# Kernel tuning notes

Measured on AMD Instinct MI355X. Metric: run time of the kernel, lower is better.

The kernel has to match this reference:

```python
import jax, jax.numpy as jnp
import numpy as np

NUM_THRESH = 1000


def setup_inputs() -> dict:
    key = jax.random.key(0)
    k1, k2 = jax.random.split(key)
    B, C, H, W = 16, 4, 512, 512
    inp = jax.random.uniform(k1, (B, C, H, W), dtype=jnp.float32)
    targ = (jax.random.uniform(k2, (B, C, H, W)) < 0.3).astype(jnp.float32)
    return {"input": inp, "target": targ}


def _max_f1_loss(input, target):
    # input, target: [B, C, H, W]; loss = mean_c (1 - max_t F1_c(t))
    B, C, H, W = input.shape
    N = B * H * W
    x = jnp.transpose(input, (1, 0, 2, 3)).reshape(C, N)   # [C, N]
    y = jnp.transpose(target, (1, 0, 2, 3)).reshape(C, N)  # [C, N]
    thresholds = jnp.linspace(0.0, 1.0, NUM_THRESH).astype(jnp.float32)

    def per_class(xc, yc):
        # idx[n] = number of thresholds strictly below xc[n]  (in [0, 1000])
        # sample n is predicted positive (xc > t_k) exactly for k < idx[n]
        idx = jnp.searchsorted(thresholds, xc, side='left')
        s_y = jax.ops.segment_sum(yc, idx, num_segments=NUM_THRESH + 1)
        s_1 = jax.ops.segment_sum(jnp.ones_like(yc), idx, num_segments=NUM_THRESH + 1)
        cum_y = jnp.cumsum(s_y)[:NUM_THRESH]  # sum of y over samples with idx <= k
        cum_1 = jnp.cumsum(s_1)[:NUM_THRESH]
        total_y = jnp.sum(yc)
        TP = total_y - cum_y            # sum(target * pred) per threshold
        PP = jnp.float32(N) - cum_1     # sum(pred) per threshold
        FP = PP - TP                    # sum((1-target) * pred)
        FN = total_y - TP               # sum(target * (1-pred))
        denom = TP + (FN + FP) * 0.5
        F1 = jnp.where(denom == 0, 0.0, TP / jnp.where(denom == 0, 1.0, denom))
        return 1.0 - jnp.max(F1)

    losses = jax.vmap(per_class)(x, y)  # [C]
    return jnp.mean(losses)


def reference(input, target):
    return _max_f1_loss(input, target)
```

## Files before the change

kernel.cpp:

```cpp
#include <hip/hip_runtime.h>

#define NBINS 1001
#define HIST_BLOCK 1024
#define ELEMS_PER_BLOCK 32768

__device__ __forceinline__ int bin_of(float v) {
    int k = (int)ceilf(v * 999.0f);
    k = (k < 0) ? 0 : k;
    k = (k > 1000) ? 1000 : k;
    return k;
}

__global__ __launch_bounds__(HIST_BLOCK, 4) void hist_kernel(
    const float* __restrict__ x, const float* __restrict__ y,
    unsigned long long* __restrict__ ghist, int HW)
{
    __shared__ unsigned int lh[2][NBINS];
    const int tid = threadIdx.x;
    if (tid < NBINS) { lh[0][tid] = 0u; lh[1][tid] = 0u; }
    __syncthreads();

    const long long start = (long long)blockIdx.x * ELEMS_PER_BLOCK;
    const int c = (int)((start / HW) & 3);

    const float4* __restrict__ x4 = (const float4*)(x + start);
    const float4* __restrict__ y4 = (const float4*)(y + start);

    unsigned int* __restrict__ h = lh[(tid >> 6) & 1];

    #pragma unroll
    for (int r = 0; r < 2; ++r) {
        float4 xv[4], yv[4];
        #pragma unroll
        for (int k = 0; k < 4; ++k) {
            const int idx = (r * 4 + k) * HIST_BLOCK + tid;
            xv[k] = x4[idx];
            yv[k] = y4[idx];
        }
        #pragma unroll
        for (int k = 0; k < 4; ++k) {
            atomicAdd(&h[bin_of(xv[k].x)], 1u + ((__float_as_uint(yv[k].x) >> 8) & 0x10000u));
            atomicAdd(&h[bin_of(xv[k].y)], 1u + ((__float_as_uint(yv[k].y) >> 8) & 0x10000u));
            atomicAdd(&h[bin_of(xv[k].z)], 1u + ((__float_as_uint(yv[k].z) >> 8) & 0x10000u));
            atomicAdd(&h[bin_of(xv[k].w)], 1u + ((__float_as_uint(yv[k].w) >> 8) & 0x10000u));
        }
    }
    __syncthreads();

    if (tid < NBINS) {
        unsigned int v = lh[0][tid] + lh[1][tid];
        if (v) {
            unsigned long long add = (unsigned long long)(v & 0xffffu)
                                   | ((unsigned long long)(v >> 16) << 32);
            atomicAdd(&ghist[(size_t)c * NBINS + tid], add);
        }
    }
}

__global__ __launch_bounds__(1024) void f1_kernel(
    const unsigned long long* __restrict__ ghist, float* __restrict__ out)
{
    __shared__ unsigned long long wtot[4][16];
    __shared__ float wmax[4][16];
    const int tid  = threadIdx.x;
    const int lane = tid & 63;
    const int wave = tid >> 6;

    unsigned long long v[4];
    #pragma unroll
    for (int c = 0; c < 4; ++c)
        v[c] = (tid < NBINS) ? ghist[(size_t)c * NBINS + tid] : 0ULL;

    #pragma unroll
    for (int off = 1; off < 64; off <<= 1) {
        #pragma unroll
        for (int c = 0; c < 4; ++c) {
            unsigned long long t = __shfl_up(v[c], off, 64);
            if (lane >= off) v[c] += t;
        }
    }
    if (lane == 63) {
        #pragma unroll
        for (int c = 0; c < 4; ++c) wtot[c][wave] = v[c];
    }
    __syncthreads();

    if (wave == 0) {
        const int c = lane >> 4, w = lane & 15;
        unsigned long long t = wtot[c][w];
        #pragma unroll
        for (int off = 1; off < 16; off <<= 1) {
            unsigned long long s = __shfl_up(t, off, 16);
            if (w >= off) t += s;
        }
        wtot[c][w] = t;
    }
    __syncthreads();

    float m[4];
    #pragma unroll
    for (int c = 0; c < 4; ++c) {
        unsigned long long cum = v[c];
        if (wave > 0) cum += wtot[c][wave - 1];
        unsigned long long tot = wtot[c][15];
        unsigned int total_cnt = (unsigned int)(tot & 0xffffffffULL);
        unsigned int total_y   = (unsigned int)(tot >> 32);
        float f1 = 0.0f;
        if (tid < NBINS - 1) {
            unsigned int cnt_cum = (unsigned int)(cum & 0xffffffffULL);
            unsigned int y_cum   = (unsigned int)(cum >> 32);
            unsigned int TP = total_y - y_cum;
            unsigned int PP = total_cnt - cnt_cum;
            unsigned int denom = total_y + PP;
            f1 = (denom == 0u) ? 0.0f : (2.0f * (float)TP) / (float)denom;
        }
        m[c] = f1;
    }

    #pragma unroll
    for (int off = 32; off > 0; off >>= 1) {
        #pragma unroll
        for (int c = 0; c < 4; ++c)
            m[c] = fmaxf(m[c], __shfl_down(m[c], off, 64));
    }
    if (lane == 0) {
        #pragma unroll
        for (int c = 0; c < 4; ++c) wmax[c][wave] = m[c];
    }
    __syncthreads();

    if (tid == 0) {
        float loss = 0.0f;
        #pragma unroll
        for (int c = 0; c < 4; ++c) {
            float mm = wmax[c][0];
            #pragma unroll
            for (int w = 1; w < 16; ++w) mm = fmaxf(mm, wmax[c][w]);
            loss += 1.0f - mm;
        }
        out[0] = loss * 0.25f;
    }
}

extern "C" void kernel_launch(void* const* d_in, const int* in_sizes, int n_in,
                              void* d_out, int out_size, void* d_ws, size_t ws_size,
                              hipStream_t stream) {
    const float* x = (const float*)d_in[0];
    const float* y = (const float*)d_in[1];
    float* out = (float*)d_out;

    const int H = 512, W = 512;
    const int HW = H * W;
    const long long total = (long long)in_sizes[0];

    unsigned long long* ghist = (unsigned long long*)d_ws;

    hipMemsetAsync(d_ws, 0, (size_t)4 * NBINS * sizeof(unsigned long long), stream);

    const int nblocks = (int)(total / ELEMS_PER_BLOCK);
    hist_kernel<<<nblocks, HIST_BLOCK, 0, stream>>>(x, y, ghist, HW);
    f1_kernel<<<1, 1024, 0, stream>>>(ghist, out);
    (void)n_in; (void)out_size; (void)ws_size;
}
```

Measured before the change: 152.5 us.

## Use smaller histogram blocks with upfront nontemporal loads and single LDS histogram

Shrinks the histogram block to 256 threads, loads all of a thread's 8 vector pairs up front with nontemporal loads before zeroing shared memory, and merges the two shared-memory histogram copies into one. The aim is to overlap global load latency with LDS initialization and to raise occupancy with more, smaller blocks. In exchange the grid has four times as many blocks, which multiplies the global 64-bit atomic flushes, and the single LDS histogram may see more atomic contention.

```diff
diff --git a/kernel.cpp b/kernel.cpp
--- a/kernel.cpp
+++ b/kernel.cpp
@@ -1,8 +1,11 @@
 #include <hip/hip_runtime.h>
 
 #define NBINS 1001
-#define HIST_BLOCK 1024
-#define ELEMS_PER_BLOCK 32768
+#define HIST_BLOCK 256
+#define VPT 8
+#define ELEMS_PER_BLOCK (HIST_BLOCK * VPT * 4)
+
+typedef float fvec4 __attribute__((ext_vector_type(4)));
 
 __device__ __forceinline__ int bin_of(float v) {
     int k = (int)ceilf(v * 999.0f);
@@ -11,48 +14,45 @@
     return k;
 }
 
-__global__ __launch_bounds__(HIST_BLOCK, 4) void hist_kernel(
+__global__ __launch_bounds__(HIST_BLOCK) void hist_kernel(
     const float* __restrict__ x, const float* __restrict__ y,
     unsigned long long* __restrict__ ghist, int HW)
 {
-    __shared__ unsigned int lh[2][NBINS];
+    __shared__ unsigned int lh[NBINS];
     const int tid = threadIdx.x;
-    if (tid < NBINS) { lh[0][tid] = 0u; lh[1][tid] = 0u; }
-    __syncthreads();
 
     const long long start = (long long)blockIdx.x * ELEMS_PER_BLOCK;
     const int c = (int)((start / HW) & 3);
 
-    const float4* __restrict__ x4 = (const float4*)(x + start);
-    const float4* __restrict__ y4 = (const float4*)(y + start);
+    const fvec4* __restrict__ x4 = (const fvec4*)(x + start);
+    const fvec4* __restrict__ y4 = (const fvec4*)(y + start);
 
-    unsigned int* __restrict__ h = lh[(tid >> 6) & 1];
+    fvec4 xv[VPT], yv[VPT];
+    #pragma unroll
+    for (int k = 0; k < VPT; ++k) {
+        const int idx = k * HIST_BLOCK + tid;
+        xv[k] = __builtin_nontemporal_load(&x4[idx]);
+        yv[k] = __builtin_nontemporal_load(&y4[idx]);
+    }
+
+    for (int i = tid; i < NBINS; i += HIST_BLOCK) lh[i] = 0u;
+    __syncthreads();
 
     #pragma unroll
-    for (int r = 0; r < 2; ++r) {
-        float4 xv[4], yv[4];
-        #pragma unroll
-        for (int k = 0; k < 4; ++k) {
-            const int idx = (r * 4 + k) * HIST_BLOCK + tid;
-            xv[k] = x4[idx];
-            yv[k] = y4[idx];
-        }
-        #pragma unroll
-        for (int k = 0; k < 4; ++k) {
-            atomicAdd(&h[bin_of(xv[k].x)], 1u + ((__float_as_uint(yv[k].x) >> 8) & 0x10000u));
-            atomicAdd(&h[bin_of(xv[k].y)], 1u + ((__float_as_uint(yv[k].y) >> 8) & 0x10000u));
-            atomicAdd(&h[bin_of(xv[k].z)], 1u + ((__float_as_uint(yv[k].z) >> 8) & 0x10000u));
-            atomicAdd(&h[bin_of(xv[k].w)], 1u + ((__float_as_uint(yv[k].w) >> 8) & 0x10000u));
-        }
+    for (int k = 0; k < VPT; ++k) {
+        atomicAdd(&lh[bin_of(xv[k].x)], 1u + ((__float_as_uint(yv[k].x) >> 8) & 0x10000u));
+        atomicAdd(&lh[bin_of(xv[k].y)], 1u + ((__float_as_uint(yv[k].y) >> 8) & 0x10000u));
+        atomicAdd(&lh[bin_of(xv[k].z)], 1u + ((__float_as_uint(yv[k].z) >> 8) & 0x10000u));
+        atomicAdd(&lh[bin_of(xv[k].w)], 1u + ((__float_as_uint(yv[k].w) >> 8) & 0x10000u));
     }
     __syncthreads();
 
-    if (tid < NBINS) {
-        unsigned int v = lh[0][tid] + lh[1][tid];
+    for (int i = tid; i < NBINS; i += HIST_BLOCK) {
+        unsigned int v = lh[i];
         if (v) {
             unsigned long long add = (unsigned long long)(v & 0xffffu)
                                    | ((unsigned long long)(v >> 16) << 32);
-            atomicAdd(&ghist[(size_t)c * NBINS + tid], add);
+            atomicAdd(&ghist[(size_t)c * NBINS + i], add);
         }
     }
 }
@@ -155,7 +155,7 @@
 
     unsigned long long* ghist = (unsigned long long*)d_ws;
 
-    hipMemsetAsync(d_ws, 0, (size_t)4 * NBINS * sizeof(unsigned long long), stream);
+    (void)hipMemsetAsync(d_ws, 0, (size_t)4 * NBINS * sizeof(unsigned long long), stream);
 
     const int nblocks = (int)(total / ELEMS_PER_BLOCK);
     hist_kernel<<<nblocks, HIST_BLOCK, 0, stream>>>(x, y, ghist, HW);
```

After: 148.0 us, median of 2. -2.9%, faster.
